# Optimization experiments

Measured on AMD Instinct MI355X. Metric: run time of the kernel, lower is better.

Reference implementation:

```python
import jax, jax.numpy as jnp
import numpy as np

VERY_NEG = -1e11
VERY_SMALL = 1e-10
PAGERANK_LAMBDA = 0.8
FACT_SCALE = 3.0


def _linear(x, W, b):
    return x @ W.T + b


def _lstm(x, Wih, Whh, bih, bhh):
    # single-layer unidirectional LSTM, pytorch gate order (i, f, g, o)
    B, T, _ = x.shape
    H = Whh.shape[1]
    def step(carry, xt):
        h, c = carry
        g = xt @ Wih.T + bih + h @ Whh.T + bhh
        i, f, gg, o = jnp.split(g, 4, axis=-1)
        c = jax.nn.sigmoid(f) * c + jax.nn.sigmoid(i) * jnp.tanh(gg)
        h = jax.nn.sigmoid(o) * jnp.tanh(c)
        return (h, c), h
    init = (jnp.zeros((B, H), x.dtype), jnp.zeros((B, H), x.dtype))
    (h_last, _), hs = jax.lax.scan(step, init, jnp.swapaxes(x, 0, 1))
    return jnp.swapaxes(hs, 0, 1), h_last


def _forward(local_entity, q2e_adj_mat, kb_fact_rel, query_text, e2f_entity, f2e_entity,
             answer_dist, word_emb, entity_emb, rel_emb, ent_W, ent_b, rel_W, rel_b,
             lstm_Wih, lstm_Whh, lstm_bih, lstm_bhh, q2e_W, q2e_b, head_W, head_b,
             tail_W, tail_b, self_W, self_b, e2e_W, e2e_b, score_W, score_b):
    B, E = local_entity.shape
    D = ent_W.shape[0]
    num_word = word_emb.shape[0] - 1
    num_entity = entity_emb.shape[0] - 1
    b_idx = jnp.arange(B)[:, None]  # (B,1) for batched gather/scatter

    # --- query LSTM encoder ---
    query_mask = (query_text != num_word).astype(jnp.float32)            # (B,Q)
    qh, q_last = _lstm(word_emb[query_text], lstm_Wih, lstm_Whh, lstm_bih, lstm_bhh)
    query_node_emb = q_last[:, None, :]                                   # (B,1,D)

    # --- fact embeddings + fact-query attention weights ---
    local_fact_emb = _linear(rel_emb[kb_fact_rel], rel_W, rel_b)          # (B,F,D)
    div = jnp.sqrt(jnp.asarray(D, jnp.float32))
    sim = jnp.einsum('bqd,bfd->bqf', qh, local_fact_emb) / div
    sim = jax.nn.softmax(sim + (1.0 - query_mask)[:, :, None] * VERY_NEG, axis=1)
    att = jnp.einsum('bqf,bqd->bfd', sim, qh)                             # (B,F,D)
    Wf = jnp.sum(att * local_fact_emb, axis=2) / div                      # (B,F)
    W_tilde = jnp.exp(Wf - jnp.max(Wf, axis=1, keepdims=True))
    # e2f_softmax[b,e] = sum of W_tilde over facts whose head is e (sparse e2f^T @ W_tilde)
    e2f_softmax = jnp.maximum(
        jnp.zeros((B, E), jnp.float32).at[b_idx, e2f_entity].add(W_tilde), VERY_SMALL)

    # --- entity embeddings (word_dim != entity_dim -> entity_linear) ---
    local_entity_emb = _linear(entity_emb[local_entity], ent_W, ent_b)    # (B,E,D)
    pagerank_f = q2e_adj_mat[:, :, 0]                                     # (B,E)

    n_layer = q2e_W.shape[0]
    for i in range(n_layer):
        q2e_emb = jnp.broadcast_to(_linear(query_node_emb, q2e_W[i], q2e_b[i]), (B, E, D))
        # entity -> fact: gather head-entity messages
        head = _linear(local_entity_emb, head_W[i], head_b[i])            # (B,E,D)
        e2f_emb = jax.nn.relu(
            _linear(local_fact_emb, self_W[i], self_b[i]) + head[b_idx, e2f_entity])
        pr = pagerank_f / e2f_softmax                                     # (B,E)
        e2f_norm = (W_tilde * pr[b_idx, e2f_entity])[:, :, None]          # (B,F,1)
        e2f_emb = e2f_emb * e2f_norm
        # fact -> entity: scatter-add to tail entities
        tail = _linear(e2f_emb, tail_W[i], tail_b[i])                     # (B,F,D)
        f2e_emb = jax.nn.relu(
            _linear(local_entity_emb, self_W[i], self_b[i])
            + jnp.zeros((B, E, D), jnp.float32).at[b_idx, f2e_entity].add(tail))
        pagerank_f = (PAGERANK_LAMBDA
                      * jnp.zeros((B, E), jnp.float32).at[b_idx, f2e_entity].add(e2f_norm[:, :, 0])
                      + (1.0 - PAGERANK_LAMBDA) * pagerank_f)
        nxt = jnp.concatenate([local_entity_emb, q2e_emb, FACT_SCALE * f2e_emb], axis=2)
        local_entity_emb = jax.nn.relu(_linear(nxt, e2e_W[i], e2e_b[i]))

    score = local_entity_emb @ score_W + score_b                          # (B,E)
    mask = (local_entity != num_entity).astype(jnp.float32)
    score = score + (1.0 - mask) * VERY_NEG
    return jax.nn.sigmoid(score) * mask


def setup_inputs() -> dict:
    key = jax.random.key(0)
    ks = jax.random.split(key, 24)
    B, E, Fc, Q = 8, 2000, 12000, 20
    WD, D = 300, 100
    NE, NW, NR, L = 100000, 40000, 300, 3
    f32 = jnp.float32
    def nrm(k, shape, scale):
        return jax.random.normal(k, shape, f32) * scale
    return {
        'local_entity': jax.random.randint(ks[0], (B, E), 0, NE),
        'q2e_adj_mat': jax.random.uniform(ks[1], (B, E, 1), f32),
        'kb_fact_rel': jax.random.randint(ks[2], (B, Fc), 0, NR),
        'query_text': jax.random.randint(ks[3], (B, Q), 0, NW),
        'e2f_entity': jax.random.randint(ks[4], (B, Fc), 0, E),
        'f2e_entity': jax.random.randint(ks[5], (B, Fc), 0, E),
        'answer_dist': jax.random.uniform(ks[6], (B, E), f32),
        'word_emb': nrm(ks[7], (NW + 1, WD), 0.02),
        'entity_emb': nrm(ks[8], (NE + 1, WD), 0.02),
        'rel_emb': nrm(ks[9], (NR + 1, 2 * WD), 0.02),
        'ent_W': nrm(ks[10], (D, WD), WD ** -0.5), 'ent_b': jnp.zeros((D,), f32),
        'rel_W': nrm(ks[11], (D, 2 * WD), (2 * WD) ** -0.5), 'rel_b': jnp.zeros((D,), f32),
        'lstm_Wih': nrm(ks[12], (4 * D, WD), WD ** -0.5),
        'lstm_Whh': nrm(ks[13], (4 * D, D), D ** -0.5),
        'lstm_bih': jnp.zeros((4 * D,), f32), 'lstm_bhh': jnp.zeros((4 * D,), f32),
        'q2e_W': nrm(ks[14], (L, D, D), D ** -0.5), 'q2e_b': jnp.zeros((L, D), f32),
        'head_W': nrm(ks[15], (L, D, D), D ** -0.5), 'head_b': jnp.zeros((L, D), f32),
        'tail_W': nrm(ks[16], (L, D, D), D ** -0.5), 'tail_b': jnp.zeros((L, D), f32),
        'self_W': nrm(ks[17], (L, D, D), D ** -0.5), 'self_b': jnp.zeros((L, D), f32),
        'e2e_W': nrm(ks[18], (L, D, 3 * D), (3 * D) ** -0.5), 'e2e_b': jnp.zeros((L, D), f32),
        'score_W': nrm(ks[19], (D,), D ** -0.5), 'score_b': jnp.zeros((), f32),
    }


def reference(local_entity, q2e_adj_mat, kb_fact_rel, query_text, e2f_entity, f2e_entity,
              answer_dist, word_emb, entity_emb, rel_emb, ent_W, ent_b, rel_W, rel_b,
              lstm_Wih, lstm_Whh, lstm_bih, lstm_bhh, q2e_W, q2e_b, head_W, head_b,
              tail_W, tail_b, self_W, self_b, e2e_W, e2e_b, score_W, score_b):
    return _forward(local_entity, q2e_adj_mat, kb_fact_rel, query_text, e2f_entity,
                    f2e_entity, answer_dist, word_emb, entity_emb, rel_emb, ent_W, ent_b,
                    rel_W, rel_b, lstm_Wih, lstm_Whh, lstm_bih, lstm_bhh, q2e_W, q2e_b,
                    head_W, head_b, tail_W, tail_b, self_W, self_b, e2e_W, e2e_b,
                    score_W, score_b)
```

## Files before the change

### kernel.cpp

```cpp
#include <hip/hip_runtime.h>
#include <math.h>

#define VERY_NEG  -100000000000.0f
#define VERY_SMALLF 1e-10f

constexpr int B  = 8;
constexpr int E  = 2000;
constexpr int FC = 12000;
constexpr int Q  = 20;
constexpr int WD = 300;
constexpr int D  = 100;
constexpr int NW = 40000;
constexpr int NE = 100000;
constexpr int G4 = 4 * D;
constexpr int NREL = 301;
constexpr int NF = B * FC;
constexpr int NR_ = B * E;
constexpr int NRP = 16384;

__device__ __forceinline__ float sigmoidf_(float x) { return 1.0f / (1.0f + expf(-x)); }

__device__ __forceinline__ void tile16(const float* __restrict__ As_, const float* __restrict__ Bs_,
                                       int rg, int cgc, float acc[4][4]) {
#pragma unroll 5
    for (int k4 = 0; k4 < 25; ++k4) {
        float a_[4][4], b_[4][4];
#pragma unroll
        for (int i = 0; i < 4; ++i) {
            float4 v = *(const float4*)&As_[(rg * 4 + i) * 104 + k4 * 4];
            a_[i][0] = v.x; a_[i][1] = v.y; a_[i][2] = v.z; a_[i][3] = v.w;
        }
#pragma unroll
        for (int kk = 0; kk < 4; ++kk) {
            float4 v = *(const float4*)&Bs_[(k4 * 4 + kk) * 100 + cgc * 4];
            b_[kk][0] = v.x; b_[kk][1] = v.y; b_[kk][2] = v.z; b_[kk][3] = v.w;
        }
#pragma unroll
        for (int kk = 0; kk < 4; ++kk)
#pragma unroll
            for (int i = 0; i < 4; ++i)
#pragma unroll
                for (int j = 0; j < 4; ++j)
                    acc[i][j] += a_[i][kk] * b_[kk][j];
    }
}

__device__ __forceinline__ void stage_B100(const float* __restrict__ Wt, int ldW, int col0, int k0,
                                           float* __restrict__ Bs_) {
    for (int i = threadIdx.x; i < 2500; i += 256) {
        int k = i / 25, d2 = i - k * 25;
        *(float4*)&Bs_[k * 100 + d2 * 4] = *(const float4*)&Wt[(size_t)(k0 + k) * ldW + col0 + d2 * 4];
    }
}

__device__ void gemm_tile_g(const float* __restrict__ A, int K,
                            const int* __restrict__ rix, int nrows,
                            const float* __restrict__ Wt, int ldW, int col0,
                            const float* __restrict__ bias,
                            float* __restrict__ C,
                            int base, float* As_, float* Bs_) {
    int tid = threadIdx.x;
    int cg_ = tid & 31, rg = tid >> 5, cgc = cg_ < 25 ? cg_ : 24;
    float acc[4][4] = {{0.f}};
    for (int k0 = 0; k0 < K; k0 += 100) {
        __syncthreads();
        for (int i = tid; i < 800; i += 256) {
            int r = i / 25, c = i - r * 25;
            int rr = base + r; if (rr >= nrows) rr = nrows - 1;
            int gr = rix ? rix[rr] : rr;
            *(float4*)&As_[r * 104 + c * 4] = *(const float4*)&A[(size_t)gr * K + k0 + c * 4];
        }
        stage_B100(Wt, ldW, col0, k0, Bs_);
        __syncthreads();
        tile16(As_, Bs_, rg, cgc, acc);
    }
    if (cg_ < 25) {
        float4 bb = *(const float4*)&bias[col0 + cg_ * 4];
#pragma unroll
        for (int i = 0; i < 4; ++i) {
            int r = base + rg * 4 + i;
            if (r < nrows) {
                float4 o;
                o.x = acc[i][0] + bb.x; o.y = acc[i][1] + bb.y;
                o.z = acc[i][2] + bb.z; o.w = acc[i][3] + bb.w;
                *(float4*)&C[(size_t)r * ldW + col0 + cg_ * 4] = o;
            }
        }
    }
}

__device__ void gemm_tile_512(const float* __restrict__ A, int K,
                              const int* __restrict__ rix, int nrows,
                              const float* __restrict__ Wt, int ldW, int col0,
                              const float* __restrict__ bias,
                              float* __restrict__ C,
                              int base, float* As_, float* Bs_) {
    int tid = threadIdx.x;
    int cg_ = tid & 31, rg = (tid >> 5) & 7, cgc = cg_ < 25 ? cg_ : 24;
    bool on = tid < 256;
    float acc[4][4] = {{0.f}};
    for (int k0 = 0; k0 < K; k0 += 100) {
        __syncthreads();
        for (int i = tid; i < 800; i += 512) {
            int r = i / 25, c = i - r * 25;
            int rr = base + r; if (rr >= nrows) rr = nrows - 1;
            int gr = rix ? rix[rr] : rr;
            *(float4*)&As_[r * 104 + c * 4] = *(const float4*)&A[(size_t)gr * K + k0 + c * 4];
        }
        for (int i = tid; i < 2500; i += 512) {
            int k = i / 25, d2 = i - k * 25;
            *(float4*)&Bs_[k * 100 + d2 * 4] = *(const float4*)&Wt[(size_t)(k0 + k) * ldW + col0 + d2 * 4];
        }
        __syncthreads();
        if (on) tile16(As_, Bs_, rg, cgc, acc);
    }
    if (on && cg_ < 25) {
        float4 bb = *(const float4*)&bias[col0 + cg_ * 4];
#pragma unroll
        for (int i = 0; i < 4; ++i) {
            int r = base + rg * 4 + i;
            if (r < nrows) {
                float4 o;
                o.x = acc[i][0] + bb.x; o.y = acc[i][1] + bb.y;
                o.z = acc[i][2] + bb.z; o.w = acc[i][3] + bb.w;
                *(float4*)&C[(size_t)r * ldW + col0 + cg_ * 4] = o;
            }
        }
    }
}

struct PrepP {
    const float *ent_W, *rel_W, *Wih, *Whh, *head_W, *self_W, *tail_W, *e2e_W, *bih, *bhh, *q2e_adj;
    float *entWt, *relWt, *WihT, *WhhT, *headWt, *selfWt, *tailWt, *e2eWt, *bihh, *pr, *e2f_sm;
    int *cnt, *present;
};

__device__ void tr_tile(const float* __restrict__ in, float* __restrict__ out, int M, int K,
                        int kx, int my, float tb[32][33]) {
    int x = threadIdx.x & 31, y = threadIdx.x >> 5;
    int k0 = kx * 32, m0 = my * 32;
    for (int yy = y; yy < 32; yy += 8) {
        int m = m0 + yy, k = k0 + x;
        if (m < M && k < K) tb[yy][x] = in[(size_t)m * K + k];
    }
    __syncthreads();
    for (int yy = y; yy < 32; yy += 8) {
        int k = k0 + yy, m = m0 + x;
        if (m < M && k < K) out[(size_t)k * M + m] = tb[x][yy];
    }
}

__global__ __launch_bounds__(256) void k_prep(PrepP p) {
    __shared__ float tb[32][33];
    int j = blockIdx.x, tid = threadIdx.x;
    if (j < 40)       { tr_tile(p.ent_W, p.entWt, 100, 300, j % 10, j / 10, tb); }
    else if (j < 116) { j -= 40;  tr_tile(p.rel_W, p.relWt, 100, 600, j % 19, j / 19, tb); }
    else if (j < 246) { j -= 116; tr_tile(p.Wih, p.WihT, 400, 300, j % 10, j / 10, tb); }
    else if (j < 298) { j -= 246; tr_tile(p.Whh, p.WhhT, 400, 100, j % 4, j / 4, tb); }
    else if (j < 346) { j -= 298; int z = j / 16, t = j % 16; tr_tile(p.head_W + z * 10000, p.headWt + z * 10000, 100, 100, t % 4, t / 4, tb); }
    else if (j < 394) { j -= 346; int z = j / 16, t = j % 16; tr_tile(p.self_W + z * 10000, p.selfWt + z * 10000, 100, 100, t % 4, t / 4, tb); }
    else if (j < 442) { j -= 394; int z = j / 16, t = j % 16; tr_tile(p.tail_W + z * 10000, p.tailWt + z * 10000, 100, 100, t % 4, t / 4, tb); }
    else if (j < 562) { j -= 442; int z = j / 40, t = j % 40; tr_tile(p.e2e_W + z * 30000, p.e2eWt + z * 30000, 100, 300, t % 10, t / 10, tb); }
    else if (j < 564) { int idx = (j - 562) * 256 + tid; if (idx < G4) p.bihh[idx] = p.bih[idx] + p.bhh[idx]; }
    else if (j < 580) { int idx = (j - 564) * 256 + tid; if (idx < 4000) ((float4*)p.pr)[idx] = ((const float4*)p.q2e_adj)[idx]; }
    else if (j < 596) { int idx = (j - 580) * 256 + tid; if (idx < 4096) ((int4*)p.cnt)[idx] = make_int4(0, 0, 0, 0); }
    else if (j < 612) { int idx = (j - 596) * 256 + tid; if (idx < 4000) ((float4*)p.e2f_sm)[idx] = make_float4(0.f, 0.f, 0.f, 0.f); }
    else              { int idx = (j - 612) * 256 + tid; if (idx < B * NREL) p.present[idx] = 0; }
}

__global__ void k_hist(const int* __restrict__ f2e, const int* __restrict__ kb_rel,
                       int* __restrict__ cnt, int* __restrict__ present) {
    int fid = blockIdx.x * 256 + threadIdx.x;
    if (fid >= NF) return;
    int b = fid / FC;
    atomicAdd(&cnt[b * E + f2e[fid]], 1);
    present[b * NREL + kb_rel[fid]] = 1;
}

struct F1P {
    const int *cnt; int *off, *cursor; float *cnt_f;
    const float *word_emb; const int *qtext; const float *WihT, *bihh; float *xW;
    const float *rel_emb, *relWt, *rel_b; float *rel_proj;
};

__device__ void scan_block(const int* __restrict__ cnt, int* __restrict__ off,
                           int* __restrict__ cursor, float* __restrict__ cnt_f, int* part) {
    int t = threadIdx.x;
    int s = 0;
    const int4* c4 = (const int4*)(cnt + t * 64);
#pragma unroll 4
    for (int i = 0; i < 16; ++i) { int4 v = c4[i]; s += v.x + v.y + v.z + v.w; }
    part[t] = s;
    __syncthreads();
    for (int d = 1; d < 256; d <<= 1) {
        int add = (t >= d) ? part[t - d] : 0;
        __syncthreads();
        part[t] += add;
        __syncthreads();
    }
    int run = part[t] - s;
    for (int i = 0; i < 64; ++i) {
        int idx = t * 64 + i;
        if (idx < NR_) {
            off[idx] = run; cursor[idx] = run; cnt_f[idx] = (float)cnt[idx];
            run += cnt[idx];
        }
    }
    if (t == 255) off[NR_] = part[255];
}

__global__ __launch_bounds__(256) void k_front1(F1P p) {
    __shared__ float smem[13328];
    int j = blockIdx.x;
    if (j == 0) {
        scan_block(p.cnt, p.off, p.cursor, p.cnt_f, (int*)smem);
    } else if (j <= 20) {
        j -= 1;
        gemm_tile_g(p.word_emb, WD, p.qtext, B * Q, p.WihT, G4, (j / 5) * 100, p.bihh,
                    p.xW, (j % 5) * 32, smem, smem + 3328);
    } else {
        j -= 21;
        gemm_tile_g(p.rel_emb, 2 * WD, nullptr, NREL, p.relWt, D, 0, p.rel_b,
                    p.rel_proj, j * 32, smem, smem + 3328);
    }
}

struct F2P {
    const float *xW, *WhhT, *q2e_W, *q2e_b; float *qh, *q2e_vec;
    const float *rel_proj, *selfWt, *self_b; float *self_proj;
};

__device__ void lstm_block(int b, const F2P& p, float* smem) {
    float* h = smem; float* c = smem + 128; float* gate = smem + 256;
    int t = threadIdx.x;
    float w[100];
    if (t < G4) {
#pragma unroll
        for (int j = 0; j < 100; ++j) w[j] = p.WhhT[j * G4 + t];
    }
    if (t < D) { h[t] = 0.f; c[t] = 0.f; }
    __syncthreads();
    for (int step = 0; step < Q; ++step) {
        if (t < G4) {
            float a0 = 0.f, a1 = 0.f, a2 = 0.f, a3 = 0.f;
#pragma unroll
            for (int k4 = 0; k4 < 25; ++k4) {
                float4 hv = *(const float4*)&h[k4 * 4];
                a0 += hv.x * w[k4 * 4 + 0];
                a1 += hv.y * w[k4 * 4 + 1];
                a2 += hv.z * w[k4 * 4 + 2];
                a3 += hv.w * w[k4 * 4 + 3];
            }
            gate[t] = p.xW[(b * Q + step) * G4 + t] + ((a0 + a1) + (a2 + a3));
        }
        __syncthreads();
        if (t < D) {
            float ig = sigmoidf_(gate[t]);
            float fg = sigmoidf_(gate[D + t]);
            float gg = tanhf(gate[2 * D + t]);
            float og = sigmoidf_(gate[3 * D + t]);
            float cn = fg * c[t] + ig * gg;
            c[t] = cn;
            float hn = og * tanhf(cn);
            h[t] = hn;
            p.qh[(b * Q + step) * D + t] = hn;
        }
        __syncthreads();
    }
    if (t < 3 * D) {
        int l = t / D, d = t - l * D;
        float acc = p.q2e_b[l * D + d];
        const float* W = p.q2e_W + (size_t)(l * D + d) * D;
        for (int k = 0; k < D; ++k) acc += h[k] * W[k];
        p.q2e_vec[(l * B + b) * D + d] = acc;
    }
}

__global__ __launch_bounds__(512) void k_front2(F2P p) {
    __shared__ float smem[13328];
    int j = blockIdx.x;
    if (j < 8) {
        lstm_block(j, p, smem);
    } else {
        j -= 8;
        int z = j / 10, t = j % 10;
        gemm_tile_512(p.rel_proj, D, nullptr, NREL, p.selfWt + z * 10000, D, 0, p.self_b + z * 100,
                      p.self_proj + (size_t)z * NREL * D, t * 32, smem, smem + 3328);
    }
}

__global__ void k_wfall(const int* __restrict__ qtext, const float* __restrict__ qh,
                        const float* __restrict__ rel_proj, const int* __restrict__ present,
                        float* __restrict__ Wt_rel) {
    __shared__ float qh_s[Q * D];
    __shared__ float msk[Q];
    __shared__ float red[512];
    int b = blockIdx.x, t = threadIdx.x;
    for (int k = t; k < Q * D; k += 320) qh_s[k] = qh[b * Q * D + k];
    if (t < Q) msk[t] = (qtext[b * Q + t] != NW) ? 1.f : 0.f;
    if (t < 192) red[320 + t] = -INFINITY;
    __syncthreads();
    float wf = 0.f;
    bool active = t < NREL;
    if (active) {
        const float* lfe = rel_proj + t * D;
        float s[Q];
#pragma unroll
        for (int q = 0; q < Q; ++q) s[q] = 0.f;
        for (int k = 0; k < D; ++k) {
            float lv = lfe[k];
#pragma unroll
            for (int q = 0; q < Q; ++q) s[q] += qh_s[q * D + k] * lv;
        }
        float m = -INFINITY;
        float sv[Q];
#pragma unroll
        for (int q = 0; q < Q; ++q) {
            s[q] *= 0.1f;
            sv[q] = s[q] + (1.f - msk[q]) * VERY_NEG;
            m = fmaxf(m, sv[q]);
        }
        float sum = 0.f;
        float ex[Q];
#pragma unroll
        for (int q = 0; q < Q; ++q) { ex[q] = expf(sv[q] - m); sum += ex[q]; }
#pragma unroll
        for (int q = 0; q < Q; ++q) wf += (ex[q] / sum) * s[q];
    }
    red[t] = (active && present[b * NREL + t]) ? wf : -INFINITY;
    __syncthreads();
    for (int st = 256; st > 0; st >>= 1) {
        if (t < st) red[t] = fmaxf(red[t], red[t + st]);
        __syncthreads();
    }
    float m = red[0];
    if (active) Wt_rel[b * NREL + t] = expf(wf - m);
}

struct MidP {
    const int *f2e, *e2f, *kb_rel; const float *Wt_rel;
    int *cursor, *sorted; float *W_tilde, *e2f_sm;
    const float *entity_emb; const int *local_entity;
    const float *entWt, *ent_b, *headWt0, *head_b0, *selfWt0, *self_b0;
    float *lee, *head, *lee_self;
};

__device__ void lee_dual_tile32(int base, const MidP& p, float* As_, float* Bs_) {
    int tid = threadIdx.x;
    int cg_ = tid & 31, rg = tid >> 5, cgc = cg_ < 25 ? cg_ : 24;
    float acc[4][4] = {{0.f}};
    for (int k0 = 0; k0 < 300; k0 += 100) {
        __syncthreads();
        for (int i = tid; i < 800; i += 256) {
            int r = i / 25, c = i - r * 25;
            int gr = p.local_entity[base + r];
            *(float4*)&As_[r * 104 + c * 4] = *(const float4*)&p.entity_emb[(size_t)gr * 300 + k0 + c * 4];
        }
        stage_B100(p.entWt, 100, 0, k0, Bs_);
        __syncthreads();
        tile16(As_, Bs_, rg, cgc, acc);
    }
    __syncthreads();
    if (cg_ < 25) {
        float4 bb = *(const float4*)&p.ent_b[cg_ * 4];
#pragma unroll
        for (int i = 0; i < 4; ++i) {
            int r = base + rg * 4 + i;
            float4 o;
            o.x = acc[i][0] + bb.x; o.y = acc[i][1] + bb.y;
            o.z = acc[i][2] + bb.z; o.w = acc[i][3] + bb.w;
            *(float4*)&p.lee[(size_t)r * 100 + cg_ * 4] = o;
            *(float4*)&As_[(rg * 4 + i) * 104 + cg_ * 4] = o;
        }
    }
    stage_B100(p.headWt0, 100, 0, 0, Bs_);
    __syncthreads();
    float acc2[4][4] = {{0.f}};
    tile16(As_, Bs_, rg, cgc, acc2);
    if (cg_ < 25) {
        float4 bb = *(const float4*)&p.head_b0[cg_ * 4];
#pragma unroll
        for (int i = 0; i < 4; ++i) {
            int r = base + rg * 4 + i;
            float4 o;
            o.x = acc2[i][0] + bb.x; o.y = acc2[i][1] + bb.y;
            o.z = acc2[i][2] + bb.z; o.w = acc2[i][3] + bb.w;
            *(float4*)&p.head[(size_t)r * 100 + cg_ * 4] = o;
        }
    }
    __syncthreads();
    stage_B100(p.selfWt0, 100, 0, 0, Bs_);
    __syncthreads();
    float acc3[4][4] = {{0.f}};
    tile16(As_, Bs_, rg, cgc, acc3);
    if (cg_ < 25) {
        float4 bb = *(const float4*)&p.self_b0[cg_ * 4];
#pragma unroll
        for (int i = 0; i < 4; ++i) {
            int r = base + rg * 4 + i;
            float4 o;
            o.x = acc3[i][0] + bb.x; o.y = acc3[i][1] + bb.y;
            o.z = acc3[i][2] + bb.z; o.w = acc3[i][3] + bb.w;
            *(float4*)&p.lee_self[(size_t)r * 100 + cg_ * 4] = o;
        }
    }
}

__global__ __launch_bounds__(256) void k_mid(MidP p) {
    __shared__ float smem[13328];
    int j = blockIdx.x, tid = threadIdx.x;
    if (j < 500) {
        lee_dual_tile32(j * 32, p, smem, smem + 3328);
    } else {
        int fid = (j - 500) * 256 + tid;
        int b = fid / FC;
        int pos = atomicAdd(&p.cursor[b * E + p.f2e[fid]], 1);
        p.sorted[pos] = fid;
        float wt = p.Wt_rel[b * NREL + p.kb_rel[fid]];
        p.W_tilde[fid] = wt;
        atomicAdd(&p.e2f_sm[b * E + p.e2f[fid]], wt);
    }
}

__global__ void k_gfact(const int* __restrict__ sorted, const int* __restrict__ kb_rel,
                        const int* __restrict__ e2f, const float* __restrict__ W_tilde,
                        const float* __restrict__ e2f_sm,
                        int* __restrict__ es_rel_s, float* __restrict__ g_s) {
    int j = blockIdx.x * 256 + threadIdx.x;
    if (j >= NF) return;
    int fid = sorted[j];
    int b = fid / FC;
    int es = e2f[fid], rel = kb_rel[fid];
    es_rel_s[j] = es | (rel << 16);
    g_s[j] = W_tilde[fid] / fmaxf(e2f_sm[b * E + es], VERY_SMALLF);
}

__global__ __launch_bounds__(256) void k_gather(const int* __restrict__ es_rel_s,
                                                const float* __restrict__ g_s,
                                                const int* __restrict__ off,
                                                const float* __restrict__ self_proj_l,
                                                const float* __restrict__ head,
                                                const float* __restrict__ pr,
                                                float* __restrict__ u, float* __restrict__ pr_acc) {
    int bid = blockIdx.x;
    int job = (bid & 7) * 500 + (bid >> 3);
    int wave = threadIdx.x >> 6, lane = threadIdx.x & 63;
    int ri = job * 4 + wave;
    int b = ri / E, bE = b * E;
    int s = off[ri], e = off[ri + 1];
    float a0 = 0.f, a1 = 0.f, ns = 0.f;
    const float* hb = head + (size_t)bE * D;
    const float* prb = pr + bE;
    for (int cs = s; cs < e; cs += 64) {
        int cnt = e - cs; if (cnt > 64) cnt = 64;
        int erl = 0; float njl = 0.f;
        if (lane < cnt) {
            erl = es_rel_s[cs + lane];
            njl = g_s[cs + lane] * prb[erl & 0xffff];
        }
        for (int j = 0; j < cnt; ++j) {
            int er = __shfl(erl, j);
            float nj = __shfl(njl, j);
            int es = er & 0xffff, rel = er >> 16;
            const float* sp = self_proj_l + rel * D;
            const float* hr = hb + (size_t)es * D;
            a0 += nj * fmaxf(0.f, sp[lane] + hr[lane]);
            if (lane < 36) a1 += nj * fmaxf(0.f, sp[lane + 64] + hr[lane + 64]);
            ns += nj;
        }
    }
    u[(size_t)ri * D + lane] = a0;
    if (lane < 36) u[(size_t)ri * D + 64 + lane] = a1;
    if (lane == 0) pr_acc[ri] = ns;
}

struct TailP {
    const float *u, *cnt_f, *tailWt_l, *tail_b_l;
    const float *cur, *lee_self_in, *q2e_l, *e2eWt_l, *e2e_b_l;
    const float *pr_acc_c; float *pr; float *nxt;
    const float *headWt_n, *head_b_n, *selfWt_n, *self_b_n;
    float *head, *lee_self_out;
    int last; const int *local_entity; const float *score_W, *score_b; float *out;
};

__global__ __launch_bounds__(256) void k_tailent(TailP p) {
    __shared__ float As_[32 * 104];
    __shared__ float Bs_[100 * 100];
    __shared__ float Fs_[32 * 104];
    int tid = threadIdx.x, base = blockIdx.x * 32;
    int cg_ = tid & 31, rg = tid >> 5, cgc = cg_ < 25 ? cg_ : 24;
    for (int i = tid; i < 800; i += 256) {
        int r = i / 25, c = i - r * 25;
        *(float4*)&As_[r * 104 + c * 4] = *(const float4*)&p.u[(size_t)(base + r) * 100 + c * 4];
    }
    stage_B100(p.tailWt_l, 100, 0, 0, Bs_);
    __syncthreads();
    float accF[4][4] = {{0.f}};
    tile16(As_, Bs_, rg, cgc, accF);
    __syncthreads();
    if (cg_ < 25) {
        float4 tbv = *(const float4*)&p.tail_b_l[cg_ * 4];
#pragma unroll
        for (int i = 0; i < 4; ++i) {
            int r = base + rg * 4 + i;
            float cf = p.cnt_f[r];
            float4 ls = *(const float4*)&p.lee_self_in[(size_t)r * 100 + cg_ * 4];
            float4 o;
            o.x = 3.f * fmaxf(0.f, ls.x + accF[i][0] + cf * tbv.x);
            o.y = 3.f * fmaxf(0.f, ls.y + accF[i][1] + cf * tbv.y);
            o.z = 3.f * fmaxf(0.f, ls.z + accF[i][2] + cf * tbv.z);
            o.w = 3.f * fmaxf(0.f, ls.w + accF[i][3] + cf * tbv.w);
            *(float4*)&Fs_[(rg * 4 + i) * 104 + cg_ * 4] = o;
        }
    }
    if (tid < 32) {
        int r = base + tid;
        p.pr[r] = 0.8f * p.pr_acc_c[r] + 0.2f * p.pr[r];
    }
    float acc[4][4] = {{0.f}};
    __syncthreads();
    for (int i = tid; i < 800; i += 256) {
        int r = i / 25, c = i - r * 25;
        *(float4*)&As_[r * 104 + c * 4] = *(const float4*)&p.cur[(size_t)(base + r) * 100 + c * 4];
    }
    stage_B100(p.e2eWt_l, 100, 0, 0, Bs_);
    __syncthreads();
    tile16(As_, Bs_, rg, cgc, acc);
    __syncthreads();
    for (int i = tid; i < 800; i += 256) {
        int r = i / 25, c = i - r * 25;
        int bb = (base + r) / E;
        *(float4*)&As_[r * 104 + c * 4] = *(const float4*)&p.q2e_l[bb * 100 + c * 4];
    }
    stage_B100(p.e2eWt_l, 100, 0, 100, Bs_);
    __syncthreads();
    tile16(As_, Bs_, rg, cgc, acc);
    __syncthreads();
    stage_B100(p.e2eWt_l, 100, 0, 200, Bs_);
    __syncthreads();
    tile16(Fs_, Bs_, rg, cgc, acc);
    __syncthreads();
    if (cg_ < 25) {
        float4 ebv = *(const float4*)&p.e2e_b_l[cg_ * 4];
#pragma unroll
        for (int i = 0; i < 4; ++i) {
            int r = base + rg * 4 + i;
            float4 o;
            o.x = fmaxf(acc[i][0] + ebv.x, 0.f); o.y = fmaxf(acc[i][1] + ebv.y, 0.f);
            o.z = fmaxf(acc[i][2] + ebv.z, 0.f); o.w = fmaxf(acc[i][3] + ebv.w, 0.f);
            *(float4*)&p.nxt[(size_t)r * 100 + cg_ * 4] = o;
            *(float4*)&As_[(rg * 4 + i) * 104 + cg_ * 4] = o;
        }
    }
    if (!p.last) {
        stage_B100(p.headWt_n, 100, 0, 0, Bs_);
        __syncthreads();
        float a2[4][4] = {{0.f}};
        tile16(As_, Bs_, rg, cgc, a2);
        if (cg_ < 25) {
            float4 bb = *(const float4*)&p.head_b_n[cg_ * 4];
#pragma unroll
            for (int i = 0; i < 4; ++i) {
                int r = base + rg * 4 + i;
                float4 o;
                o.x = a2[i][0] + bb.x; o.y = a2[i][1] + bb.y;
                o.z = a2[i][2] + bb.z; o.w = a2[i][3] + bb.w;
                *(float4*)&p.head[(size_t)r * 100 + cg_ * 4] = o;
            }
        }
        __syncthreads();
        stage_B100(p.selfWt_n, 100, 0, 0, Bs_);
        __syncthreads();
        float a3[4][4] = {{0.f}};
        tile16(As_, Bs_, rg, cgc, a3);
        if (cg_ < 25) {
            float4 bb = *(const float4*)&p.self_b_n[cg_ * 4];
#pragma unroll
            for (int i = 0; i < 4; ++i) {
                int r = base + rg * 4 + i;
                float4 o;
                o.x = a3[i][0] + bb.x; o.y = a3[i][1] + bb.y;
                o.z = a3[i][2] + bb.z; o.w = a3[i][3] + bb.w;
                *(float4*)&p.lee_self_out[(size_t)r * 100 + cg_ * 4] = o;
            }
        }
    } else {
        __syncthreads();
        if (tid < 32) {
            int r = base + tid;
            if (p.local_entity[r] == NE) { p.out[r] = 0.f; }
            else {
                float a = p.score_b[0];
                for (int k = 0; k < D; ++k) a += As_[tid * 104 + k] * p.score_W[k];
                p.out[r] = 1.f / (1.f + expf(-a));
            }
        }
    }
}

extern "C" void kernel_launch(void* const* d_in, const int* in_sizes, int n_in,
                              void* d_out, int out_size, void* d_ws, size_t ws_size,
                              hipStream_t stream) {
    const int*   local_entity = (const int*)d_in[0];
    const float* q2e_adj      = (const float*)d_in[1];
    const int*   kb_rel       = (const int*)d_in[2];
    const int*   qtext        = (const int*)d_in[3];
    const int*   e2f          = (const int*)d_in[4];
    const int*   f2e          = (const int*)d_in[5];
    const float* word_emb     = (const float*)d_in[7];
    const float* entity_emb   = (const float*)d_in[8];
    const float* rel_emb      = (const float*)d_in[9];
    const float* ent_W        = (const float*)d_in[10];
    const float* ent_b        = (const float*)d_in[11];
    const float* rel_W        = (const float*)d_in[12];
    const float* rel_b        = (const float*)d_in[13];
    const float* lstm_Wih     = (const float*)d_in[14];
    const float* lstm_Whh     = (const float*)d_in[15];
    const float* lstm_bih     = (const float*)d_in[16];
    const float* lstm_bhh     = (const float*)d_in[17];
    const float* q2e_W        = (const float*)d_in[18];
    const float* q2e_b        = (const float*)d_in[19];
    const float* head_W       = (const float*)d_in[20];
    const float* head_b       = (const float*)d_in[21];
    const float* tail_W       = (const float*)d_in[22];
    const float* tail_b       = (const float*)d_in[23];
    const float* self_W       = (const float*)d_in[24];
    const float* self_b       = (const float*)d_in[25];
    const float* e2e_W        = (const float*)d_in[26];
    const float* e2e_b        = (const float*)d_in[27];
    const float* score_W      = (const float*)d_in[28];
    const float* score_b      = (const float*)d_in[29];

    float* ws = (float*)d_ws;
    float* rel_proj  = ws;
    float* self_proj = rel_proj  + NREL * D;
    float* xW        = self_proj + 3 * NREL * D;
    float* qh        = xW        + B * Q * G4;
    float* q2e_vec   = qh        + B * Q * D;
    float* Wt_rel    = q2e_vec   + 3 * B * D;
    float* W_tilde   = Wt_rel    + B * NREL;
    float* e2f_sm    = W_tilde   + NF;
    float* leeA      = e2f_sm    + NR_;
    float* leeB      = leeA      + NR_ * D;
    float* head      = leeB      + NR_ * D;
    float* lee_self  = head      + NR_ * D;
    float* u_buf     = lee_self  + NR_ * D;
    float* pr        = u_buf     + NR_ * D;
    float* pr_acc    = pr        + NR_;
    float* cnt_f     = pr_acc    + NR_;
    float* g_s       = cnt_f     + NR_;
    float* entWt     = g_s       + NF;
    float* relWt     = entWt     + WD * D;
    float* WihT      = relWt     + 2 * WD * D;
    float* WhhT      = WihT      + WD * G4;
    float* headWt    = WhhT      + D * G4;
    float* selfWt    = headWt    + 3 * D * D;
    float* tailWt    = selfWt    + 3 * D * D;
    float* e2eWt     = tailWt    + 3 * D * D;
    float* bihh      = e2eWt     + 9 * D * D;
    int*   present   = (int*)(bihh + G4);
    int*   cnt       = present   + B * NREL;
    int*   cursor    = cnt       + NRP;
    int*   off       = cursor    + NR_;
    int*   sorted    = off       + NR_ + 1;
    int*   es_rel_s  = sorted    + NF;

    PrepP pp;
    pp.ent_W = ent_W; pp.rel_W = rel_W; pp.Wih = lstm_Wih; pp.Whh = lstm_Whh;
    pp.head_W = head_W; pp.self_W = self_W; pp.tail_W = tail_W; pp.e2e_W = e2e_W;
    pp.bih = lstm_bih; pp.bhh = lstm_bhh; pp.q2e_adj = q2e_adj;
    pp.entWt = entWt; pp.relWt = relWt; pp.WihT = WihT; pp.WhhT = WhhT;
    pp.headWt = headWt; pp.selfWt = selfWt; pp.tailWt = tailWt; pp.e2eWt = e2eWt;
    pp.bihh = bihh; pp.pr = pr; pp.e2f_sm = e2f_sm; pp.cnt = cnt; pp.present = present;
    k_prep<<<615, 256, 0, stream>>>(pp);

    k_hist<<<375, 256, 0, stream>>>(f2e, kb_rel, cnt, present);

    F1P f1;
    f1.cnt = cnt; f1.off = off; f1.cursor = cursor; f1.cnt_f = cnt_f;
    f1.word_emb = word_emb; f1.qtext = qtext; f1.WihT = WihT; f1.bihh = bihh; f1.xW = xW;
    f1.rel_emb = rel_emb; f1.relWt = relWt; f1.rel_b = rel_b; f1.rel_proj = rel_proj;
    k_front1<<<31, 256, 0, stream>>>(f1);

    F2P f2;
    f2.xW = xW; f2.WhhT = WhhT; f2.q2e_W = q2e_W; f2.q2e_b = q2e_b;
    f2.qh = qh; f2.q2e_vec = q2e_vec;
    f2.rel_proj = rel_proj; f2.selfWt = selfWt; f2.self_b = self_b; f2.self_proj = self_proj;
    k_front2<<<38, 512, 0, stream>>>(f2);

    k_wfall<<<B, 320, 0, stream>>>(qtext, qh, rel_proj, present, Wt_rel);

    MidP mp;
    mp.f2e = f2e; mp.e2f = e2f; mp.kb_rel = kb_rel; mp.Wt_rel = Wt_rel;
    mp.cursor = cursor; mp.sorted = sorted; mp.W_tilde = W_tilde; mp.e2f_sm = e2f_sm;
    mp.entity_emb = entity_emb; mp.local_entity = local_entity;
    mp.entWt = entWt; mp.ent_b = ent_b;
    mp.headWt0 = headWt; mp.head_b0 = head_b; mp.selfWt0 = selfWt; mp.self_b0 = self_b;
    mp.lee = leeA; mp.head = head; mp.lee_self = lee_self;
    k_mid<<<500 + 375, 256, 0, stream>>>(mp);

    k_gfact<<<375, 256, 0, stream>>>(sorted, kb_rel, e2f, W_tilde, e2f_sm, es_rel_s, g_s);

    float* cur = leeA; float* nxt = leeB;
    for (int l = 0; l < 3; ++l) {
        k_gather<<<4000, 256, 0, stream>>>(es_rel_s, g_s, off, self_proj + (size_t)l * NREL * D,
                                           head, pr, u_buf, pr_acc);
        TailP tp;
        tp.u = u_buf; tp.cnt_f = cnt_f;
        tp.tailWt_l = tailWt + l * 10000; tp.tail_b_l = tail_b + l * 100;
        tp.cur = cur; tp.lee_self_in = lee_self; tp.q2e_l = q2e_vec + l * B * D;
        tp.e2eWt_l = e2eWt + l * 30000; tp.e2e_b_l = e2e_b + l * 100;
        tp.pr_acc_c = pr_acc; tp.pr = pr; tp.nxt = nxt;
        int ln = (l < 2) ? l + 1 : l;
        tp.headWt_n = headWt + ln * 10000; tp.head_b_n = head_b + ln * 100;
        tp.selfWt_n = selfWt + ln * 10000; tp.self_b_n = self_b + ln * 100;
        tp.head = head; tp.lee_self_out = lee_self;
        tp.last = (l == 2); tp.local_entity = local_entity;
        tp.score_W = score_W; tp.score_b = score_b; tp.out = (float*)d_out;
        k_tailent<<<NR_ / 32, 256, 0, stream>>>(tp);
        float* t = cur; cur = nxt; nxt = t;
    }
}
```

Before: 348.2 us.

## Merge histogram into prep kernel, fuse wfall into LSTM, move entity GEMMs earlier

The fact histogram moves into the prep kernel, and the cnt/present zeroing is replaced by a hipMemsetAsync. The fact-attention (wfall) computation now runs inside the LSTM block using shared-memory qh, so the qh global buffer and a separate launch go away. The entity embedding and head/self projection tiles move from the mid kernel into front1, so they overlap with the small query GEMMs, and the scatter part becomes its own kernel. The aim is fewer launches and better overlap of independent work; the cost is more per-block work and higher register pressure in the LSTM block.

Result: faster. 321.8 us (-7.6%).

```diff
diff --git a/kernel.cpp b/kernel.cpp
--- a/kernel.cpp
+++ b/kernel.cpp
@@ -129,10 +129,10 @@
     }
 }
 
-struct PrepP {
+struct P0 {
     const float *ent_W, *rel_W, *Wih, *Whh, *head_W, *self_W, *tail_W, *e2e_W, *bih, *bhh, *q2e_adj;
     float *entWt, *relWt, *WihT, *WhhT, *headWt, *selfWt, *tailWt, *e2eWt, *bihh, *pr, *e2f_sm;
-    int *cnt, *present;
+    const int *f2e, *kb_rel; int *cnt, *present;
 };
 
 __device__ void tr_tile(const float* __restrict__ in, float* __restrict__ out, int M, int K,
@@ -150,7 +150,7 @@
     }
 }
 
-__global__ __launch_bounds__(256) void k_prep(PrepP p) {
+__global__ __launch_bounds__(256) void k_prep0(P0 p) {
     __shared__ float tb[32][33];
     int j = blockIdx.x, tid = threadIdx.x;
     if (j < 40)       { tr_tile(p.ent_W, p.entWt, 100, 300, j % 10, j / 10, tb); }
@@ -163,24 +163,22 @@
     else if (j < 562) { j -= 442; int z = j / 40, t = j % 40; tr_tile(p.e2e_W + z * 30000, p.e2eWt + z * 30000, 100, 300, t % 10, t / 10, tb); }
     else if (j < 564) { int idx = (j - 562) * 256 + tid; if (idx < G4) p.bihh[idx] = p.bih[idx] + p.bhh[idx]; }
     else if (j < 580) { int idx = (j - 564) * 256 + tid; if (idx < 4000) ((float4*)p.pr)[idx] = ((const float4*)p.q2e_adj)[idx]; }
-    else if (j < 596) { int idx = (j - 580) * 256 + tid; if (idx < 4096) ((int4*)p.cnt)[idx] = make_int4(0, 0, 0, 0); }
-    else if (j < 612) { int idx = (j - 596) * 256 + tid; if (idx < 4000) ((float4*)p.e2f_sm)[idx] = make_float4(0.f, 0.f, 0.f, 0.f); }
-    else              { int idx = (j - 612) * 256 + tid; if (idx < B * NREL) p.present[idx] = 0; }
-}
-
-__global__ void k_hist(const int* __restrict__ f2e, const int* __restrict__ kb_rel,
-                       int* __restrict__ cnt, int* __restrict__ present) {
-    int fid = blockIdx.x * 256 + threadIdx.x;
-    if (fid >= NF) return;
-    int b = fid / FC;
-    atomicAdd(&cnt[b * E + f2e[fid]], 1);
-    present[b * NREL + kb_rel[fid]] = 1;
+    else if (j < 596) { int idx = (j - 580) * 256 + tid; if (idx < 4000) ((float4*)p.e2f_sm)[idx] = make_float4(0.f, 0.f, 0.f, 0.f); }
+    else {
+        int fid = (j - 596) * 256 + tid;
+        int b = fid / FC;
+        atomicAdd(&p.cnt[b * E + p.f2e[fid]], 1);
+        p.present[b * NREL + p.kb_rel[fid]] = 1;
+    }
 }
 
 struct F1P {
     const int *cnt; int *off, *cursor; float *cnt_f;
     const float *word_emb; const int *qtext; const float *WihT, *bihh; float *xW;
     const float *rel_emb, *relWt, *rel_b; float *rel_proj;
+    const float *entity_emb; const int *local_entity;
+    const float *entWt, *ent_b, *headWt0, *head_b0, *selfWt0, *self_b0;
+    float *lee, *head, *lee_self;
 };
 
 __device__ void scan_block(const int* __restrict__ cnt, int* __restrict__ off,
@@ -207,6 +205,67 @@
         }
     }
     if (t == 255) off[NR_] = part[255];
+}
+
+__device__ void lee_dual_tile32(int base, const F1P& p, float* As_, float* Bs_) {
+    int tid = threadIdx.x;
+    int cg_ = tid & 31, rg = tid >> 5, cgc = cg_ < 25 ? cg_ : 24;
+    float acc[4][4] = {{0.f}};
+    for (int k0 = 0; k0 < 300; k0 += 100) {
+        __syncthreads();
+        for (int i = tid; i < 800; i += 256) {
+            int r = i / 25, c = i - r * 25;
+            int gr = p.local_entity[base + r];
+            *(float4*)&As_[r * 104 + c * 4] = *(const float4*)&p.entity_emb[(size_t)gr * 300 + k0 + c * 4];
+        }
+        stage_B100(p.entWt, 100, 0, k0, Bs_);
+        __syncthreads();
+        tile16(As_, Bs_, rg, cgc, acc);
+    }
+    __syncthreads();
+    if (cg_ < 25) {
+        float4 bb = *(const float4*)&p.ent_b[cg_ * 4];
+#pragma unroll
+        for (int i = 0; i < 4; ++i) {
+            int r = base + rg * 4 + i;
+            float4 o;
+            o.x = acc[i][0] + bb.x; o.y = acc[i][1] + bb.y;
+            o.z = acc[i][2] + bb.z; o.w = acc[i][3] + bb.w;
+            *(float4*)&p.lee[(size_t)r * 100 + cg_ * 4] = o;
+            *(float4*)&As_[(rg * 4 + i) * 104 + cg_ * 4] = o;
+        }
+    }
+    stage_B100(p.headWt0, 100, 0, 0, Bs_);
+    __syncthreads();
+    float acc2[4][4] = {{0.f}};
+    tile16(As_, Bs_, rg, cgc, acc2);
+    if (cg_ < 25) {
+        float4 bb = *(const float4*)&p.head_b0[cg_ * 4];
+#pragma unroll
+        for (int i = 0; i < 4; ++i) {
+            int r = base + rg * 4 + i;
+            float4 o;
+            o.x = acc2[i][0] + bb.x; o.y = acc2[i][1] + bb.y;
+            o.z = acc2[i][2] + bb.z; o.w = acc2[i][3] + bb.w;
+            *(float4*)&p.head[(size_t)r * 100 + cg_ * 4] = o;
+        }
+    }
+    __syncthreads();
+    stage_B100(p.selfWt0, 100, 0, 0, Bs_);
+    __syncthreads();
+    float acc3[4][4] = {{0.f}};
+    tile16(As_, Bs_, rg, cgc, acc3);
+    if (cg_ < 25) {
+        float4 bb = *(const float4*)&p.self_b0[cg_ * 4];
+#pragma unroll
+        for (int i = 0; i < 4; ++i) {
+            int r = base + rg * 4 + i;
+            float4 o;
+            o.x = acc3[i][0] + bb.x; o.y = acc3[i][1] + bb.y;
+            o.z = acc3[i][2] + bb.z; o.w = acc3[i][3] + bb.w;
+            *(float4*)&p.lee_self[(size_t)r * 100 + cg_ * 4] = o;
+        }
+    }
 }
 
 __global__ __launch_bounds__(256) void k_front1(F1P p) {
@@ -218,20 +277,29 @@
         j -= 1;
         gemm_tile_g(p.word_emb, WD, p.qtext, B * Q, p.WihT, G4, (j / 5) * 100, p.bihh,
                     p.xW, (j % 5) * 32, smem, smem + 3328);
-    } else {
+    } else if (j <= 30) {
         j -= 21;
         gemm_tile_g(p.rel_emb, 2 * WD, nullptr, NREL, p.relWt, D, 0, p.rel_b,
                     p.rel_proj, j * 32, smem, smem + 3328);
+    } else {
+        lee_dual_tile32((j - 31) * 32, p, smem, smem + 3328);
     }
 }
 
 struct F2P {
-    const float *xW, *WhhT, *q2e_W, *q2e_b; float *qh, *q2e_vec;
-    const float *rel_proj, *selfWt, *self_b; float *self_proj;
+    const float *xW, *WhhT, *q2e_W, *q2e_b; float *q2e_vec;
+    const int *qtext, *present;
+    const float *rel_proj; float *Wt_rel;
+    const float *selfWt, *self_b; float *self_proj;
 };
 
-__device__ void lstm_block(int b, const F2P& p, float* smem) {
-    float* h = smem; float* c = smem + 128; float* gate = smem + 256;
+__device__ void lstm_wfall_block(int b, const F2P& p, float* smem) {
+    float* h    = smem;
+    float* c    = smem + 128;
+    float* gate = smem + 256;
+    float* qh_s = smem + 704;
+    float* msk  = smem + 2704;
+    float* red  = smem + 2752;
     int t = threadIdx.x;
     float w[100];
     if (t < G4) {
@@ -239,6 +307,7 @@
         for (int j = 0; j < 100; ++j) w[j] = p.WhhT[j * G4 + t];
     }
     if (t < D) { h[t] = 0.f; c[t] = 0.f; }
+    if (t < Q) msk[t] = (p.qtext[b * Q + t] != NW) ? 1.f : 0.f;
     __syncthreads();
     for (int step = 0; step < Q; ++step) {
         if (t < G4) {
@@ -263,7 +332,7 @@
             c[t] = cn;
             float hn = og * tanhf(cn);
             h[t] = hn;
-            p.qh[(b * Q + step) * D + t] = hn;
+            qh_s[step * D + t] = hn;
         }
         __syncthreads();
     }
@@ -274,13 +343,47 @@
         for (int k = 0; k < D; ++k) acc += h[k] * W[k];
         p.q2e_vec[(l * B + b) * D + d] = acc;
     }
+    float wf = 0.f;
+    bool active = t < NREL;
+    if (active) {
+        const float* lfe = p.rel_proj + t * D;
+        float s[Q];
+#pragma unroll
+        for (int q = 0; q < Q; ++q) s[q] = 0.f;
+        for (int k = 0; k < D; ++k) {
+            float lv = lfe[k];
+#pragma unroll
+            for (int q = 0; q < Q; ++q) s[q] += qh_s[q * D + k] * lv;
+        }
+        float m = -INFINITY;
+        float sv[Q];
+#pragma unroll
+        for (int q = 0; q < Q; ++q) {
+            s[q] *= 0.1f;
+            sv[q] = s[q] + (1.f - msk[q]) * VERY_NEG;
+            m = fmaxf(m, sv[q]);
+        }
+        float sum = 0.f;
+        float ex[Q];
+#pragma unroll
+        for (int q = 0; q < Q; ++q) { ex[q] = expf(sv[q] - m); sum += ex[q]; }
+#pragma unroll
+        for (int q = 0; q < Q; ++q) wf += (ex[q] / sum) * s[q];
+    }
+    red[t] = (active && p.present[b * NREL + t]) ? wf : -INFINITY;
+    __syncthreads();
+    for (int st = 256; st > 0; st >>= 1) {
+        if (t < st) red[t] = fmaxf(red[t], red[t + st]);
+        __syncthreads();
+    }
+    if (active) p.Wt_rel[b * NREL + t] = expf(wf - red[0]);
 }
 
 __global__ __launch_bounds__(512) void k_front2(F2P p) {
     __shared__ float smem[13328];
     int j = blockIdx.x;
     if (j < 8) {
-        lstm_block(j, p, smem);
+        lstm_wfall_block(j, p, smem);
     } else {
         j -= 8;
         int z = j / 10, t = j % 10;
@@ -289,137 +392,17 @@
     }
 }
 
-__global__ void k_wfall(const int* __restrict__ qtext, const float* __restrict__ qh,
-                        const float* __restrict__ rel_proj, const int* __restrict__ present,
-                        float* __restrict__ Wt_rel) {
-    __shared__ float qh_s[Q * D];
-    __shared__ float msk[Q];
-    __shared__ float red[512];
-    int b = blockIdx.x, t = threadIdx.x;
-    for (int k = t; k < Q * D; k += 320) qh_s[k] = qh[b * Q * D + k];
-    if (t < Q) msk[t] = (qtext[b * Q + t] != NW) ? 1.f : 0.f;
-    if (t < 192) red[320 + t] = -INFINITY;
-    __syncthreads();
-    float wf = 0.f;
-    bool active = t < NREL;
-    if (active) {
-        const float* lfe = rel_proj + t * D;
-        float s[Q];
-#pragma unroll
-        for (int q = 0; q < Q; ++q) s[q] = 0.f;
-        for (int k = 0; k < D; ++k) {
-            float lv = lfe[k];
-#pragma unroll
-            for (int q = 0; q < Q; ++q) s[q] += qh_s[q * D + k] * lv;
-        }
-        float m = -INFINITY;
-        float sv[Q];
-#pragma unroll
-        for (int q = 0; q < Q; ++q) {
-            s[q] *= 0.1f;
-            sv[q] = s[q] + (1.f - msk[q]) * VERY_NEG;
-            m = fmaxf(m, sv[q]);
-        }
-        float sum = 0.f;
-        float ex[Q];
-#pragma unroll
-        for (int q = 0; q < Q; ++q) { ex[q] = expf(sv[q] - m); sum += ex[q]; }
-#pragma unroll
-        for (int q = 0; q < Q; ++q) wf += (ex[q] / sum) * s[q];
-    }
-    red[t] = (active && present[b * NREL + t]) ? wf : -INFINITY;
-    __syncthreads();
-    for (int st = 256; st > 0; st >>= 1) {
-        if (t < st) red[t] = fmaxf(red[t], red[t + st]);
-        __syncthreads();
-    }
-    float m = red[0];
-    if (active) Wt_rel[b * NREL + t] = expf(wf - m);
-}
-
-struct MidP {
-    const int *f2e, *e2f, *kb_rel; const float *Wt_rel;
-    int *cursor, *sorted; float *W_tilde, *e2f_sm;
-    const float *entity_emb; const int *local_entity;
-    const float *entWt, *ent_b, *headWt0, *head_b0, *selfWt0, *self_b0;
-    float *lee, *head, *lee_self;
-};
-
-__device__ void lee_dual_tile32(int base, const MidP& p, float* As_, float* Bs_) {
-    int tid = threadIdx.x;
-    int cg_ = tid & 31, rg = tid >> 5, cgc = cg_ < 25 ? cg_ : 24;
-    float acc[4][4] = {{0.f}};
-    for (int k0 = 0; k0 < 300; k0 += 100) {
-        __syncthreads();
-        for (int i = tid; i < 800; i += 256) {
-            int r = i / 25, c = i - r * 25;
-            int gr = p.local_entity[base + r];
-            *(float4*)&As_[r * 104 + c * 4] = *(const float4*)&p.entity_emb[(size_t)gr * 300 + k0 + c * 4];
-        }
-        stage_B100(p.entWt, 100, 0, k0, Bs_);
-        __syncthreads();
-        tile16(As_, Bs_, rg, cgc, acc);
-    }
-    __syncthreads();
-    if (cg_ < 25) {
-        float4 bb = *(const float4*)&p.ent_b[cg_ * 4];
-#pragma unroll
-        for (int i = 0; i < 4; ++i) {
-            int r = base + rg * 4 + i;
-            float4 o;
-            o.x = acc[i][0] + bb.x; o.y = acc[i][1] + bb.y;
-            o.z = acc[i][2] + bb.z; o.w = acc[i][3] + bb.w;
-            *(float4*)&p.lee[(size_t)r * 100 + cg_ * 4] = o;
-            *(float4*)&As_[(rg * 4 + i) * 104 + cg_ * 4] = o;
-        }
-    }
-    stage_B100(p.headWt0, 100, 0, 0, Bs_);
-    __syncthreads();
-    float acc2[4][4] = {{0.f}};
-    tile16(As_, Bs_, rg, cgc, acc2);
-    if (cg_ < 25) {
-        float4 bb = *(const float4*)&p.head_b0[cg_ * 4];
-#pragma unroll
-        for (int i = 0; i < 4; ++i) {
-            int r = base + rg * 4 + i;
-            float4 o;
-            o.x = acc2[i][0] + bb.x; o.y = acc2[i][1] + bb.y;
-            o.z = acc2[i][2] + bb.z; o.w = acc2[i][3] + bb.w;
-            *(float4*)&p.head[(size_t)r * 100 + cg_ * 4] = o;
-        }
-    }
-    __syncthreads();
-    stage_B100(p.selfWt0, 100, 0, 0, Bs_);
-    __syncthreads();
-    float acc3[4][4] = {{0.f}};
-    tile16(As_, Bs_, rg, cgc, acc3);
-    if (cg_ < 25) {
-        float4 bb = *(const float4*)&p.self_b0[cg_ * 4];
-#pragma unroll
-        for (int i = 0; i < 4; ++i) {
-            int r = base + rg * 4 + i;
-            float4 o;
-            o.x = acc3[i][0] + bb.x; o.y = acc3[i][1] + bb.y;
-            o.z = acc3[i][2] + bb.z; o.w = acc3[i][3] + bb.w;
-            *(float4*)&p.lee_self[(size_t)r * 100 + cg_ * 4] = o;
-        }
-    }
-}
-
-__global__ __launch_bounds__(256) void k_mid(MidP p) {
-    __shared__ float smem[13328];
-    int j = blockIdx.x, tid = threadIdx.x;
-    if (j < 500) {
-        lee_dual_tile32(j * 32, p, smem, smem + 3328);
-    } else {
-        int fid = (j - 500) * 256 + tid;
-        int b = fid / FC;
-        int pos = atomicAdd(&p.cursor[b * E + p.f2e[fid]], 1);
-        p.sorted[pos] = fid;
-        float wt = p.Wt_rel[b * NREL + p.kb_rel[fid]];
-        p.W_tilde[fid] = wt;
-        atomicAdd(&p.e2f_sm[b * E + p.e2f[fid]], wt);
-    }
+__global__ void k_scef(const int* __restrict__ f2e, const int* __restrict__ e2f,
+                       const int* __restrict__ kb_rel, const float* __restrict__ Wt_rel,
+                       int* __restrict__ cursor, int* __restrict__ sorted,
+                       float* __restrict__ W_tilde, float* __restrict__ e2f_sm) {
+    int fid = blockIdx.x * 256 + threadIdx.x;
+    int b = fid / FC;
+    int pos = atomicAdd(&cursor[b * E + f2e[fid]], 1);
+    sorted[pos] = fid;
+    float wt = Wt_rel[b * NREL + kb_rel[fid]];
+    W_tilde[fid] = wt;
+    atomicAdd(&e2f_sm[b * E + e2f[fid]], wt);
 }
 
 __global__ void k_gfact(const int* __restrict__ sorted, const int* __restrict__ kb_rel,
@@ -635,8 +618,7 @@
     float* rel_proj  = ws;
     float* self_proj = rel_proj  + NREL * D;
     float* xW        = self_proj + 3 * NREL * D;
-    float* qh        = xW        + B * Q * G4;
-    float* q2e_vec   = qh        + B * Q * D;
+    float* q2e_vec   = xW        + B * Q * G4;
     float* Wt_rel    = q2e_vec   + 3 * B * D;
     float* W_tilde   = Wt_rel    + B * NREL;
     float* e2f_sm    = W_tilde   + NF;
@@ -665,40 +647,36 @@
     int*   sorted    = off       + NR_ + 1;
     int*   es_rel_s  = sorted    + NF;
 
-    PrepP pp;
-    pp.ent_W = ent_W; pp.rel_W = rel_W; pp.Wih = lstm_Wih; pp.Whh = lstm_Whh;
-    pp.head_W = head_W; pp.self_W = self_W; pp.tail_W = tail_W; pp.e2e_W = e2e_W;
-    pp.bih = lstm_bih; pp.bhh = lstm_bhh; pp.q2e_adj = q2e_adj;
-    pp.entWt = entWt; pp.relWt = relWt; pp.WihT = WihT; pp.WhhT = WhhT;
-    pp.headWt = headWt; pp.selfWt = selfWt; pp.tailWt = tailWt; pp.e2eWt = e2eWt;
-    pp.bihh = bihh; pp.pr = pr; pp.e2f_sm = e2f_sm; pp.cnt = cnt; pp.present = present;
-    k_prep<<<615, 256, 0, stream>>>(pp);
-
-    k_hist<<<375, 256, 0, stream>>>(f2e, kb_rel, cnt, present);
+    hipMemsetAsync(present, 0, (size_t)(B * NREL + NRP) * sizeof(int), stream);
+
+    P0 p0;
+    p0.ent_W = ent_W; p0.rel_W = rel_W; p0.Wih = lstm_Wih; p0.Whh = lstm_Whh;
+    p0.head_W = head_W; p0.self_W = self_W; p0.tail_W = tail_W; p0.e2e_W = e2e_W;
+    p0.bih = lstm_bih; p0.bhh = lstm_bhh; p0.q2e_adj = q2e_adj;
+    p0.entWt = entWt; p0.relWt = relWt; p0.WihT = WihT; p0.WhhT = WhhT;
+    p0.headWt = headWt; p0.selfWt = selfWt; p0.tailWt = tailWt; p0.e2eWt = e2eWt;
+    p0.bihh = bihh; p0.pr = pr; p0.e2f_sm = e2f_sm;
+    p0.f2e = f2e; p0.kb_rel = kb_rel; p0.cnt = cnt; p0.present = present;
+    k_prep0<<<971, 256, 0, stream>>>(p0);
 
     F1P f1;
     f1.cnt = cnt; f1.off = off; f1.cursor = cursor; f1.cnt_f = cnt_f;
     f1.word_emb = word_emb; f1.qtext = qtext; f1.WihT = WihT; f1.bihh = bihh; f1.xW = xW;
     f1.rel_emb = rel_emb; f1.relWt = relWt; f1.rel_b = rel_b; f1.rel_proj = rel_proj;
-    k_front1<<<31, 256, 0, stream>>>(f1);
+    f1.entity_emb = entity_emb; f1.local_entity = local_entity;
+    f1.entWt = entWt; f1.ent_b = ent_b;
+    f1.headWt0 = headWt; f1.head_b0 = head_b; f1.selfWt0 = selfWt; f1.self_b0 = self_b;
+    f1.lee = leeA; f1.head = head; f1.lee_self = lee_self;
+    k_front1<<<531, 256, 0, stream>>>(f1);
 
     F2P f2;
-    f2.xW = xW; f2.WhhT = WhhT; f2.q2e_W = q2e_W; f2.q2e_b = q2e_b;
-    f2.qh = qh; f2.q2e_vec = q2e_vec;
-    f2.rel_proj = rel_proj; f2.selfWt = selfWt; f2.self_b = self_b; f2.self_proj = self_proj;
+    f2.xW = xW; f2.WhhT = WhhT; f2.q2e_W = q2e_W; f2.q2e_b = q2e_b; f2.q2e_vec = q2e_vec;
+    f2.qtext = qtext; f2.present = present;
+    f2.rel_proj = rel_proj; f2.Wt_rel = Wt_rel;
+    f2.selfWt = selfWt; f2.self_b = self_b; f2.self_proj = self_proj;
     k_front2<<<38, 512, 0, stream>>>(f2);
 
-    k_wfall<<<B, 320, 0, stream>>>(qtext, qh, rel_proj, present, Wt_rel);
-
-    MidP mp;
-    mp.f2e = f2e; mp.e2f = e2f; mp.kb_rel = kb_rel; mp.Wt_rel = Wt_rel;
-    mp.cursor = cursor; mp.sorted = sorted; mp.W_tilde = W_tilde; mp.e2f_sm = e2f_sm;
-    mp.entity_emb = entity_emb; mp.local_entity = local_entity;
-    mp.entWt = entWt; mp.ent_b = ent_b;
-    mp.headWt0 = headWt; mp.head_b0 = head_b; mp.selfWt0 = selfWt; mp.self_b0 = self_b;
-    mp.lee = leeA; mp.head = head; mp.lee_self = lee_self;
-    k_mid<<<500 + 375, 256, 0, stream>>>(mp);
-
+    k_scef<<<375, 256, 0, stream>>>(f2e, e2f, kb_rel, Wt_rel, cursor, sorted, W_tilde, e2f_sm);
     k_gfact<<<375, 256, 0, stream>>>(sorted, kb_rel, e2f, W_tilde, e2f_sm, es_rel_s, g_s);
 
     float* cur = leeA; float* nxt = leeB;
@@ -717,7 +695,7 @@
         tp.head = head; tp.lee_self_out = lee_self;
         tp.last = (l == 2); tp.local_entity = local_entity;
         tp.score_W = score_W; tp.score_b = score_b; tp.out = (float*)d_out;
-        k_tailent<<<NR_ / 32, 256, 0, stream>>>(tp);
+        k_tailent<<<500, 256, 0, stream>>>(tp);
         float* t = cur; cur = nxt; nxt = t;
     }
 }
```
